# Kernel optimization log

Hardware: AMD Instinct MI355X
Metric: run time of the kernel (lower is better)

## Reference

```python
import jax, jax.numpy as jnp
import numpy as np

B, H, W, C = 2, 64, 64, 256
NH, K = 8, 7
HD = C // NH


def setup_inputs() -> dict:
    key = jax.random.key(0)
    ks = jax.random.split(key, 5)
    s = lambda fan: 1.0 / np.sqrt(fan)
    return {
        "x": jax.random.normal(ks[0], (B, H, W, C), jnp.float32),
        "ln1_w": jnp.ones((C,), jnp.float32),
        "ln1_b": jnp.zeros((C,), jnp.float32),
        "qkv_w": jax.random.normal(ks[1], (3 * C, C), jnp.float32) * s(C),
        "qkv_b": jnp.zeros((3 * C,), jnp.float32),
        "proj_w": jax.random.normal(ks[2], (C, C), jnp.float32) * s(C),
        "proj_b": jnp.zeros((C,), jnp.float32),
        "ln2_w": jnp.ones((C,), jnp.float32),
        "ln2_b": jnp.zeros((C,), jnp.float32),
        "fc1_w": jax.random.normal(ks[3], (4 * C, C), jnp.float32) * s(C),
        "fc1_b": jnp.zeros((4 * C,), jnp.float32),
        "fc2_w": jax.random.normal(ks[4], (C, 4 * C), jnp.float32) * s(4 * C),
        "fc2_b": jnp.zeros((C,), jnp.float32),
    }


def _ln(x, w, b, eps=1e-5):
    m = x.mean(-1, keepdims=True)
    v = ((x - m) ** 2).mean(-1, keepdims=True)
    return (x - m) * jax.lax.rsqrt(v + eps) * w + b


def _nbr_idx(n, k):
    # NATTEN non-causal window: start clamped so the full k-window fits in [0, n)
    half = k // 2
    start = np.clip(np.arange(n) - half, 0, n - k)
    return jnp.asarray(start[:, None] + np.arange(k)[None, :])  # [n, k]


def reference(x, ln1_w, ln1_b, qkv_w, qkv_b, proj_w, proj_b,
              ln2_w, ln2_b, fc1_w, fc1_b, fc2_w, fc2_b):
    shortcut = x
    xn = _ln(x, ln1_w, ln1_b)
    qkv = (xn @ qkv_w.T + qkv_b).reshape(B, H, W, 3, NH, HD)
    qkv = jnp.transpose(qkv, (3, 0, 4, 1, 2, 5))  # [3,B,NH,H,W,HD]
    q, k, v = qkv[0], qkv[1], qkv[2]
    q = q * (HD ** -0.5)
    ih = _nbr_idx(H, K)[:, None, :, None]   # [H,1,K,1]
    iw = _nbr_idx(W, K)[None, :, None, :]   # [1,W,1,K]
    # gather 7x7 neighborhoods -> [B,NH,H,W,K,K,HD] -> [B,NH,H,W,K*K,HD]
    k_nb = k[:, :, ih, iw, :].reshape(B, NH, H, W, K * K, HD)
    v_nb = v[:, :, ih, iw, :].reshape(B, NH, H, W, K * K, HD)
    attn = jnp.einsum("bnijd,bnijkd->bnijk", q, k_nb)  # na2d_qk
    attn = jax.nn.softmax(attn, axis=-1)
    out = jnp.einsum("bnijk,bnijkd->bnijd", attn, v_nb)  # na2d_av
    out = jnp.transpose(out, (0, 2, 3, 1, 4)).reshape(B, H, W, C)
    out = out @ proj_w.T + proj_b
    x = shortcut + out
    h = _ln(x, ln2_w, ln2_b)
    h = jax.nn.gelu(h @ fc1_w.T + fc1_b, approximate=False)
    h = h @ fc2_w.T + fc2_b
    return x + h
```

## Files before the change

kernel.cpp:

```cpp
#include <hip/hip_runtime.h>
#include <math.h>

#define Hdim 64
#define Wdim 64
#define NTOK 8192

typedef unsigned short ushortT;
typedef __attribute__((ext_vector_type(8))) short short8;
typedef __attribute__((ext_vector_type(4))) float floatx4;

__device__ inline ushortT f2bf(float x) {
    union { float f; unsigned u; } v; v.f = x;
    unsigned r = (v.u + 0x7fffu + ((v.u >> 16) & 1u)) >> 16;
    return (ushortT)r;
}

#define GLOAD_LDS16(g, l) __builtin_amdgcn_global_load_lds( \
    (const __attribute__((address_space(1))) unsigned int*)(g), \
    (__attribute__((address_space(3))) unsigned int*)(l), 16, 0, 0)

__global__ __launch_bounds__(256) void convert_weights(
        const float* __restrict__ qkv_w, const float* __restrict__ proj_w,
        const float* __restrict__ fc1_w, const float* __restrict__ fc2_w,
        ushortT* __restrict__ o_qkv, ushortT* __restrict__ o_proj,
        ushortT* __restrict__ o_fc1, ushortT* __restrict__ o_fc2) {
    int idx = blockIdx.x * 256 + threadIdx.x;
    const float* src; ushortT* dst; int local;
    if (idx < 49152)        { src = qkv_w;  dst = o_qkv;  local = idx; }
    else if (idx < 65536)   { src = proj_w; dst = o_proj; local = idx - 49152; }
    else if (idx < 131072)  { src = fc1_w;  dst = o_fc1;  local = idx - 65536; }
    else                    { src = fc2_w;  dst = o_fc2;  local = idx - 131072; }
    float4 v = ((const float4*)src)[local];
    ushortT o[4] = {f2bf(v.x), f2bf(v.y), f2bf(v.z), f2bf(v.w)};
    *(uint2*)(dst + (size_t)local * 4) = *(uint2*)o;
}

__global__ __launch_bounds__(256) void ln_v2(const float* __restrict__ x,
                                             const float* __restrict__ w,
                                             const float* __restrict__ b,
                                             ushortT* __restrict__ y) {
    int wave = threadIdx.x >> 6, lane = threadIdx.x & 63;
    int t = blockIdx.x * 4 + wave;
    float4 v = *(const float4*)(x + (size_t)t * 256 + lane * 4);
    float s = v.x + v.y + v.z + v.w;
    float sq = v.x * v.x + v.y * v.y + v.z * v.z + v.w * v.w;
#pragma unroll
    for (int off = 32; off > 0; off >>= 1) {
        s  += __shfl_xor(s, off, 64);
        sq += __shfl_xor(sq, off, 64);
    }
    float mean = s * (1.0f / 256.0f);
    float var  = sq * (1.0f / 256.0f) - mean * mean;
    float r = rsqrtf(var + 1e-5f);
    float4 wv = *(const float4*)(w + lane * 4);
    float4 bv = *(const float4*)(b + lane * 4);
    ushortT o[4] = {f2bf((v.x - mean) * r * wv.x + bv.x),
                    f2bf((v.y - mean) * r * wv.y + bv.y),
                    f2bf((v.z - mean) * r * wv.z + bv.z),
                    f2bf((v.w - mean) * r * wv.w + bv.w)};
    *(uint2*)(y + (size_t)t * 256 + lane * 4) = *(uint2*)o;
}

template <int EPI>
__global__ __launch_bounds__(256) void gemm_bf16_v2(const ushortT* __restrict__ A,
                                                    const ushortT* __restrict__ Bw,
                                                    const float* __restrict__ bias,
                                                    const float* __restrict__ res,
                                                    void* __restrict__ out0,
                                                    ushortT* __restrict__ kb,
                                                    ushortT* __restrict__ vb,
                                                    int N, int K) {
    __shared__ ushortT As[64 * 64];
    __shared__ ushortT Bs[64 * 64];
    const int tid  = threadIdx.x;
    const int wave = tid >> 6, lane = tid & 63;
    const int wm = wave >> 1, wn = wave & 1;
    const int ln16 = lane & 15, kg = lane >> 4;
    const int m0 = blockIdx.y * 64, n0 = blockIdx.x * 64;
    const int g8 = (((lane & 7) ^ (lane >> 3)) * 8);
    const int srow = wave * 16 + (lane >> 3);

    const floatx4 fzero = {0.f, 0.f, 0.f, 0.f};
    floatx4 acc[2][2];
#pragma unroll
    for (int i = 0; i < 2; ++i)
#pragma unroll
        for (int j = 0; j < 2; ++j) acc[i][j] = fzero;

    for (int kt = 0; kt < K; kt += 64) {
#pragma unroll
        for (int p = 0; p < 2; ++p) {
            int row = srow + p * 8;
            GLOAD_LDS16(A  + (size_t)(m0 + row) * K + kt + g8, As + wave * 1024 + p * 512);
            GLOAD_LDS16(Bw + (size_t)(n0 + row) * K + kt + g8, Bs + wave * 1024 + p * 512);
        }
        __syncthreads();
#pragma unroll
        for (int s = 0; s < 2; ++s) {
            short8 a[2], b[2];
#pragma unroll
            for (int i = 0; i < 2; ++i) {
                int ra = wm * 32 + i * 16 + ln16;
                a[i] = *(const short8*)(As + ra * 64 + (((s * 4 + kg) ^ (ra & 7)) * 8));
            }
#pragma unroll
            for (int j = 0; j < 2; ++j) {
                int rb = wn * 32 + j * 16 + ln16;
                b[j] = *(const short8*)(Bs + rb * 64 + (((s * 4 + kg) ^ (rb & 7)) * 8));
            }
#pragma unroll
            for (int i = 0; i < 2; ++i)
#pragma unroll
                for (int j = 0; j < 2; ++j)
                    acc[i][j] = __builtin_amdgcn_mfma_f32_16x16x32_bf16(a[i], b[j], acc[i][j], 0, 0, 0);
        }
        __syncthreads();
    }

#pragma unroll
    for (int j = 0; j < 2; ++j) {
        int col = n0 + wn * 32 + j * 16 + ln16;
        float bsv = bias[col];
        if (EPI == 0) {
            int part = col >> 8, h = (col >> 5) & 7, d = col & 31;
            ushortT* dst = part == 0 ? (ushortT*)out0 : (part == 1 ? kb : vb);
            float scl = part == 0 ? 0.17677669529663687f : 1.0f;
#pragma unroll
            for (int i = 0; i < 2; ++i)
#pragma unroll
                for (int r = 0; r < 4; ++r) {
                    int row = m0 + wm * 32 + i * 16 + kg * 4 + r;
                    int bI = row >> 12, tin = row & 4095;
                    dst[((size_t)(bI * 8 + h) * 4096 + tin) * 32 + d] =
                        f2bf((acc[i][j][r] + bsv) * scl);
                }
        } else {
#pragma unroll
            for (int i = 0; i < 2; ++i)
#pragma unroll
                for (int r = 0; r < 4; ++r) {
                    int row = m0 + wm * 32 + i * 16 + kg * 4 + r;
                    float v = acc[i][j][r] + bsv;
                    if (EPI == 1) {
                        v += res[(size_t)row * N + col];
                        ((float*)out0)[(size_t)row * N + col] = v;
                    } else {
                        v = 0.5f * v * (1.0f + erff(v * 0.70710678118654752f));
                        ((ushortT*)out0)[(size_t)row * N + col] = f2bf(v);
                    }
                }
        }
    }
}

__global__ __launch_bounds__(256) void natten_v3(const ushortT* __restrict__ qb,
                                                 const ushortT* __restrict__ kb,
                                                 const ushortT* __restrict__ vb,
                                                 ushortT* __restrict__ attn_out) {
    __shared__ ushortT KVs[2 * 196 * 40];
    __shared__ float Ps[64][52];
    ushortT* Ks = KVs;
    ushortT* Vs = KVs + 196 * 40;
    const int tid = threadIdx.x, bid = blockIdx.x;
    const int tile = bid & 63, h = (bid >> 6) & 7, b = bid >> 9;
    const int ti = tile >> 3, tj = tile & 7;
    const int r0 = min(max(ti * 8 - 3, 0), Hdim - 14);
    const int c0 = min(max(tj * 8 - 3, 0), Wdim - 14);
    const size_t base = (size_t)(b * 8 + h) * 4096 * 32;

    for (int idx = tid; idx < 1568; idx += 256) {
        int t = idx;
        const ushortT* src = kb;
        ushortT* dst = Ks;
        if (t >= 784) { t -= 784; src = vb; dst = Vs; }
        int pos = t >> 2, ch = t & 3;
        int dr = pos / 14, dc = pos - dr * 14;
        int tok = (r0 + dr) * 64 + (c0 + dc);
        *(uint4*)(dst + pos * 40 + ch * 8) = *(const uint4*)(src + base + (size_t)tok * 32 + ch * 8);
    }

    const int tl = tid >> 2, s = tid & 3;
    const int i = ti * 8 + (tl >> 3), j = tj * 8 + (tl & 7);
    const int si = min(max(i - 3, 0), Hdim - 7), sj = min(max(j - 3, 0), Wdim - 7);
    const int lbase = (si - r0) * 14 + (sj - c0);
    const int tin = i * 64 + j;

    float q[32];
    {
        const ushortT* qp = qb + base + (size_t)tin * 32;
#pragma unroll
        for (int c4 = 0; c4 < 4; ++c4) {
            uint4 u = *(const uint4*)(qp + c4 * 8);
            unsigned uu[4] = {u.x, u.y, u.z, u.w};
#pragma unroll
            for (int e = 0; e < 4; ++e) {
                union { unsigned v; float f; } lo, hi;
                lo.v = uu[e] << 16; hi.v = uu[e] & 0xffff0000u;
                q[c4 * 8 + e * 2] = lo.f; q[c4 * 8 + e * 2 + 1] = hi.f;
            }
        }
    }
    __syncthreads();

    float sc[13];
#pragma unroll
    for (int cI = 0; cI < 13; ++cI) {
        int n = s + cI * 4;
        if (n < 49) {
            int di = n / 7, dj = n - di * 7;
            const ushortT* kr = Ks + (lbase + di * 14 + dj) * 40;
            float a = 0.f;
#pragma unroll
            for (int c4 = 0; c4 < 4; ++c4) {
                uint4 u = *(const uint4*)(kr + c4 * 8);
                unsigned uu[4] = {u.x, u.y, u.z, u.w};
#pragma unroll
                for (int e = 0; e < 4; ++e) {
                    union { unsigned v; float f; } lo, hi;
                    lo.v = uu[e] << 16; hi.v = uu[e] & 0xffff0000u;
                    a += q[c4 * 8 + e * 2] * lo.f + q[c4 * 8 + e * 2 + 1] * hi.f;
                }
            }
            sc[cI] = a;
        }
    }
    float m = -1e30f;
#pragma unroll
    for (int cI = 0; cI < 13; ++cI) if (s + cI * 4 < 49) m = fmaxf(m, sc[cI]);
    m = fmaxf(m, __shfl_xor(m, 1, 64));
    m = fmaxf(m, __shfl_xor(m, 2, 64));
    float tot = 0.f;
#pragma unroll
    for (int cI = 0; cI < 13; ++cI) if (s + cI * 4 < 49) { sc[cI] = __expf(sc[cI] - m); tot += sc[cI]; }
    tot += __shfl_xor(tot, 1, 64);
    tot += __shfl_xor(tot, 2, 64);
    float inv = 1.0f / tot;
#pragma unroll
    for (int cI = 0; cI < 13; ++cI) if (s + cI * 4 < 49) Ps[tl][s + cI * 4] = sc[cI] * inv;
    __syncthreads();

    float o[8] = {0.f, 0.f, 0.f, 0.f, 0.f, 0.f, 0.f, 0.f};
#pragma unroll
    for (int n = 0; n < 49; ++n) {
        int di = n / 7, dj = n - di * 7;
        float p = Ps[tl][n];
        const ushortT* vr = Vs + (lbase + di * 14 + dj) * 40 + s * 8;
        uint4 u = *(const uint4*)vr;
        unsigned uu[4] = {u.x, u.y, u.z, u.w};
#pragma unroll
        for (int e = 0; e < 4; ++e) {
            union { unsigned v; float f; } lo, hi;
            lo.v = uu[e] << 16; hi.v = uu[e] & 0xffff0000u;
            o[e * 2]     += p * lo.f;
            o[e * 2 + 1] += p * hi.f;
        }
    }
    unsigned up[4];
#pragma unroll
    for (int d = 0; d < 4; ++d)
        up[d] = (unsigned)f2bf(o[2 * d]) | ((unsigned)f2bf(o[2 * d + 1]) << 16);
    size_t tq = (size_t)(b * 4096 + tin);
    *(uint4*)(attn_out + tq * 256 + h * 32 + s * 8) = make_uint4(up[0], up[1], up[2], up[3]);
}

extern "C" void kernel_launch(void* const* d_in, const int* in_sizes, int n_in,
                              void* d_out, int out_size, void* d_ws, size_t ws_size,
                              hipStream_t stream) {
    const float* x      = (const float*)d_in[0];
    const float* ln1_w  = (const float*)d_in[1];
    const float* ln1_b  = (const float*)d_in[2];
    const float* qkv_w  = (const float*)d_in[3];
    const float* qkv_b  = (const float*)d_in[4];
    const float* proj_w = (const float*)d_in[5];
    const float* proj_b = (const float*)d_in[6];
    const float* ln2_w  = (const float*)d_in[7];
    const float* ln2_b  = (const float*)d_in[8];
    const float* fc1_w  = (const float*)d_in[9];
    const float* fc1_b  = (const float*)d_in[10];
    const float* fc2_w  = (const float*)d_in[11];
    const float* fc2_b  = (const float*)d_in[12];
    float* out = (float*)d_out;

    char* ws = (char*)d_ws;
    size_t off = 0;
    ushortT* wqkv = (ushortT*)(ws + off); off += (size_t)196608 * 2;
    ushortT* wproj= (ushortT*)(ws + off); off += (size_t)65536 * 2;
    ushortT* wfc1 = (ushortT*)(ws + off); off += (size_t)262144 * 2;
    ushortT* wfc2 = (ushortT*)(ws + off); off += (size_t)262144 * 2;
    ushortT* xn   = (ushortT*)(ws + off); off += (size_t)NTOK * 256 * 2;
    ushortT* qbuf = (ushortT*)(ws + off); off += (size_t)NTOK * 256 * 2;
    ushortT* kbuf = (ushortT*)(ws + off); off += (size_t)NTOK * 256 * 2;
    ushortT* vbuf = (ushortT*)(ws + off); off += (size_t)NTOK * 256 * 2;
    ushortT* attn = (ushortT*)(ws + off); off += (size_t)NTOK * 256 * 2;
    float*   x2   = (float*)  (ws + off); off += (size_t)NTOK * 256 * 4;
    ushortT* hb   = (ushortT*)(ws + off); off += (size_t)NTOK * 256 * 2;
    ushortT* h1   = (ushortT*)(ws + off); off += (size_t)NTOK * 1024 * 2;

    dim3 blk(256);
    convert_weights<<<768, blk, 0, stream>>>(qkv_w, proj_w, fc1_w, fc2_w,
                                             wqkv, wproj, wfc1, wfc2);
    ln_v2<<<2048, blk, 0, stream>>>(x, ln1_w, ln1_b, xn);
    gemm_bf16_v2<0><<<dim3(12, 128), blk, 0, stream>>>(xn, wqkv, qkv_b, nullptr,
                                                       qbuf, kbuf, vbuf, 768, 256);
    natten_v3<<<1024, blk, 0, stream>>>(qbuf, kbuf, vbuf, attn);
    gemm_bf16_v2<1><<<dim3(4, 128), blk, 0, stream>>>(attn, wproj, proj_b, x,
                                                      x2, nullptr, nullptr, 256, 256);
    ln_v2<<<2048, blk, 0, stream>>>(x2, ln2_w, ln2_b, hb);
    gemm_bf16_v2<2><<<dim3(16, 128), blk, 0, stream>>>(hb, wfc1, fc1_b, nullptr,
                                                       h1, nullptr, nullptr, 1024, 256);
    gemm_bf16_v2<1><<<dim3(4, 128), blk, 0, stream>>>(h1, wfc2, fc2_b, x2,
                                                      out, nullptr, nullptr, 256, 1024);
}
```

Baseline: 153.7 us.

## Enlarge GEMM tiles to 128x128 and fuse weight conversion with first LayerNorm

The bf16 GEMM now uses 128x128 block tiles, with each wave computing a 64x64 sub-tile through 4x4 MFMA accumulators. This raises operand reuse per LDS load and cuts the number of blocks. Weight conversion and LN1 are merged into a single launch to save one kernel launch. The larger tile cuts grid sizes to as few as 128 blocks, which may leave CUs idle on the smaller GEMMs, and it increases register pressure.

```diff
diff --git a/kernel.cpp b/kernel.cpp
--- a/kernel.cpp
+++ b/kernel.cpp
@@ -19,20 +19,45 @@
     (const __attribute__((address_space(1))) unsigned int*)(g), \
     (__attribute__((address_space(3))) unsigned int*)(l), 16, 0, 0)
 
-__global__ __launch_bounds__(256) void convert_weights(
+__global__ __launch_bounds__(256) void prep_kernel(
         const float* __restrict__ qkv_w, const float* __restrict__ proj_w,
         const float* __restrict__ fc1_w, const float* __restrict__ fc2_w,
         ushortT* __restrict__ o_qkv, ushortT* __restrict__ o_proj,
-        ushortT* __restrict__ o_fc1, ushortT* __restrict__ o_fc2) {
-    int idx = blockIdx.x * 256 + threadIdx.x;
-    const float* src; ushortT* dst; int local;
-    if (idx < 49152)        { src = qkv_w;  dst = o_qkv;  local = idx; }
-    else if (idx < 65536)   { src = proj_w; dst = o_proj; local = idx - 49152; }
-    else if (idx < 131072)  { src = fc1_w;  dst = o_fc1;  local = idx - 65536; }
-    else                    { src = fc2_w;  dst = o_fc2;  local = idx - 131072; }
-    float4 v = ((const float4*)src)[local];
-    ushortT o[4] = {f2bf(v.x), f2bf(v.y), f2bf(v.z), f2bf(v.w)};
-    *(uint2*)(dst + (size_t)local * 4) = *(uint2*)o;
+        ushortT* __restrict__ o_fc1, ushortT* __restrict__ o_fc2,
+        const float* __restrict__ x, const float* __restrict__ ln1_w,
+        const float* __restrict__ ln1_b, ushortT* __restrict__ xn) {
+    if (blockIdx.x < 768) {
+        int idx = blockIdx.x * 256 + threadIdx.x;
+        const float* src; ushortT* dst; int local;
+        if (idx < 49152)        { src = qkv_w;  dst = o_qkv;  local = idx; }
+        else if (idx < 65536)   { src = proj_w; dst = o_proj; local = idx - 49152; }
+        else if (idx < 131072)  { src = fc1_w;  dst = o_fc1;  local = idx - 65536; }
+        else                    { src = fc2_w;  dst = o_fc2;  local = idx - 131072; }
+        float4 v = ((const float4*)src)[local];
+        ushortT o[4] = {f2bf(v.x), f2bf(v.y), f2bf(v.z), f2bf(v.w)};
+        *(uint2*)(dst + (size_t)local * 4) = *(uint2*)o;
+    } else {
+        int wave = threadIdx.x >> 6, lane = threadIdx.x & 63;
+        int t = (blockIdx.x - 768) * 4 + wave;
+        float4 v = *(const float4*)(x + (size_t)t * 256 + lane * 4);
+        float s = v.x + v.y + v.z + v.w;
+        float sq = v.x * v.x + v.y * v.y + v.z * v.z + v.w * v.w;
+#pragma unroll
+        for (int off = 32; off > 0; off >>= 1) {
+            s  += __shfl_xor(s, off, 64);
+            sq += __shfl_xor(sq, off, 64);
+        }
+        float mean = s * (1.0f / 256.0f);
+        float var  = sq * (1.0f / 256.0f) - mean * mean;
+        float r = rsqrtf(var + 1e-5f);
+        float4 wv = *(const float4*)(ln1_w + lane * 4);
+        float4 bv = *(const float4*)(ln1_b + lane * 4);
+        ushortT o[4] = {f2bf((v.x - mean) * r * wv.x + bv.x),
+                        f2bf((v.y - mean) * r * wv.y + bv.y),
+                        f2bf((v.z - mean) * r * wv.z + bv.z),
+                        f2bf((v.w - mean) * r * wv.w + bv.w)};
+        *(uint2*)(xn + (size_t)t * 256 + lane * 4) = *(uint2*)o;
+    }
 }
 
 __global__ __launch_bounds__(256) void ln_v2(const float* __restrict__ x,
@@ -62,7 +87,7 @@
 }
 
 template <int EPI>
-__global__ __launch_bounds__(256) void gemm_bf16_v2(const ushortT* __restrict__ A,
+__global__ __launch_bounds__(256) void gemm_bf16_v3(const ushortT* __restrict__ A,
                                                     const ushortT* __restrict__ Bw,
                                                     const float* __restrict__ bias,
                                                     const float* __restrict__ res,
@@ -70,76 +95,79 @@
                                                     ushortT* __restrict__ kb,
                                                     ushortT* __restrict__ vb,
                                                     int N, int K) {
-    __shared__ ushortT As[64 * 64];
-    __shared__ ushortT Bs[64 * 64];
+    __shared__ ushortT As[128 * 64];
+    __shared__ ushortT Bs[128 * 64];
     const int tid  = threadIdx.x;
     const int wave = tid >> 6, lane = tid & 63;
     const int wm = wave >> 1, wn = wave & 1;
     const int ln16 = lane & 15, kg = lane >> 4;
-    const int m0 = blockIdx.y * 64, n0 = blockIdx.x * 64;
-    const int g8 = (((lane & 7) ^ (lane >> 3)) * 8);
-    const int srow = wave * 16 + (lane >> 3);
+    const int m0 = blockIdx.y * 128, n0 = blockIdx.x * 128;
+
+    const int srow = tid >> 3;
+    const int spos = tid & 7;
+    const int sgc  = spos ^ (srow & 7);
 
     const floatx4 fzero = {0.f, 0.f, 0.f, 0.f};
-    floatx4 acc[2][2];
-#pragma unroll
-    for (int i = 0; i < 2; ++i)
-#pragma unroll
-        for (int j = 0; j < 2; ++j) acc[i][j] = fzero;
+    floatx4 acc[4][4];
+#pragma unroll
+    for (int i = 0; i < 4; ++i)
+#pragma unroll
+        for (int j = 0; j < 4; ++j) acc[i][j] = fzero;
 
     for (int kt = 0; kt < K; kt += 64) {
 #pragma unroll
-        for (int p = 0; p < 2; ++p) {
-            int row = srow + p * 8;
-            GLOAD_LDS16(A  + (size_t)(m0 + row) * K + kt + g8, As + wave * 1024 + p * 512);
-            GLOAD_LDS16(Bw + (size_t)(n0 + row) * K + kt + g8, Bs + wave * 1024 + p * 512);
+        for (int q = 0; q < 4; ++q) {
+            int row = q * 32 + srow;
+            GLOAD_LDS16(A  + (size_t)(m0 + row) * K + kt + sgc * 8, As + (q * 256 + tid - lane) * 8);
+            GLOAD_LDS16(Bw + (size_t)(n0 + row) * K + kt + sgc * 8, Bs + (q * 256 + tid - lane) * 8);
         }
         __syncthreads();
 #pragma unroll
         for (int s = 0; s < 2; ++s) {
-            short8 a[2], b[2];
-#pragma unroll
-            for (int i = 0; i < 2; ++i) {
-                int ra = wm * 32 + i * 16 + ln16;
-                a[i] = *(const short8*)(As + ra * 64 + (((s * 4 + kg) ^ (ra & 7)) * 8));
+            int c = s * 4 + kg;
+            short8 a[4], b[4];
+#pragma unroll
+            for (int i = 0; i < 4; ++i) {
+                int ra = wm * 64 + i * 16 + ln16;
+                a[i] = *(const short8*)(As + ra * 64 + ((c ^ (ra & 7)) * 8));
             }
 #pragma unroll
-            for (int j = 0; j < 2; ++j) {
-                int rb = wn * 32 + j * 16 + ln16;
-                b[j] = *(const short8*)(Bs + rb * 64 + (((s * 4 + kg) ^ (rb & 7)) * 8));
+            for (int j = 0; j < 4; ++j) {
+                int rb = wn * 64 + j * 16 + ln16;
+                b[j] = *(const short8*)(Bs + rb * 64 + ((c ^ (rb & 7)) * 8));
             }
 #pragma unroll
-            for (int i = 0; i < 2; ++i)
-#pragma unroll
-                for (int j = 0; j < 2; ++j)
+            for (int i = 0; i < 4; ++i)
+#pragma unroll
+                for (int j = 0; j < 4; ++j)
                     acc[i][j] = __builtin_amdgcn_mfma_f32_16x16x32_bf16(a[i], b[j], acc[i][j], 0, 0, 0);
         }
         __syncthreads();
     }
 
 #pragma unroll
-    for (int j = 0; j < 2; ++j) {
-        int col = n0 + wn * 32 + j * 16 + ln16;
+    for (int j = 0; j < 4; ++j) {
+        int col = n0 + wn * 64 + j * 16 + ln16;
         float bsv = bias[col];
         if (EPI == 0) {
             int part = col >> 8, h = (col >> 5) & 7, d = col & 31;
             ushortT* dst = part == 0 ? (ushortT*)out0 : (part == 1 ? kb : vb);
             float scl = part == 0 ? 0.17677669529663687f : 1.0f;
 #pragma unroll
-            for (int i = 0; i < 2; ++i)
+            for (int i = 0; i < 4; ++i)
 #pragma unroll
                 for (int r = 0; r < 4; ++r) {
-                    int row = m0 + wm * 32 + i * 16 + kg * 4 + r;
+                    int row = m0 + wm * 64 + i * 16 + kg * 4 + r;
                     int bI = row >> 12, tin = row & 4095;
                     dst[((size_t)(bI * 8 + h) * 4096 + tin) * 32 + d] =
                         f2bf((acc[i][j][r] + bsv) * scl);
                 }
         } else {
 #pragma unroll
-            for (int i = 0; i < 2; ++i)
+            for (int i = 0; i < 4; ++i)
 #pragma unroll
                 for (int r = 0; r < 4; ++r) {
-                    int row = m0 + wm * 32 + i * 16 + kg * 4 + r;
+                    int row = m0 + wm * 64 + i * 16 + kg * 4 + r;
                     float v = acc[i][j][r] + bsv;
                     if (EPI == 1) {
                         v += res[(size_t)row * N + col];
@@ -297,17 +325,17 @@
     ushortT* h1   = (ushortT*)(ws + off); off += (size_t)NTOK * 1024 * 2;
 
     dim3 blk(256);
-    convert_weights<<<768, blk, 0, stream>>>(qkv_w, proj_w, fc1_w, fc2_w,
-                                             wqkv, wproj, wfc1, wfc2);
-    ln_v2<<<2048, blk, 0, stream>>>(x, ln1_w, ln1_b, xn);
-    gemm_bf16_v2<0><<<dim3(12, 128), blk, 0, stream>>>(xn, wqkv, qkv_b, nullptr,
-                                                       qbuf, kbuf, vbuf, 768, 256);
+    prep_kernel<<<2816, blk, 0, stream>>>(qkv_w, proj_w, fc1_w, fc2_w,
+                                          wqkv, wproj, wfc1, wfc2,
+                                          x, ln1_w, ln1_b, xn);
+    gemm_bf16_v3<0><<<dim3(6, 64), blk, 0, stream>>>(xn, wqkv, qkv_b, nullptr,
+                                                     qbuf, kbuf, vbuf, 768, 256);
     natten_v3<<<1024, blk, 0, stream>>>(qbuf, kbuf, vbuf, attn);
-    gemm_bf16_v2<1><<<dim3(4, 128), blk, 0, stream>>>(attn, wproj, proj_b, x,
-                                                      x2, nullptr, nullptr, 256, 256);
+    gemm_bf16_v3<1><<<dim3(2, 64), blk, 0, stream>>>(attn, wproj, proj_b, x,
+                                                     x2, nullptr, nullptr, 256, 256);
     ln_v2<<<2048, blk, 0, stream>>>(x2, ln2_w, ln2_b, hb);
-    gemm_bf16_v2<2><<<dim3(16, 128), blk, 0, stream>>>(hb, wfc1, fc1_b, nullptr,
-                                                       h1, nullptr, nullptr, 1024, 256);
-    gemm_bf16_v2<1><<<dim3(4, 128), blk, 0, stream>>>(h1, wfc2, fc2_b, x2,
-                                                      out, nullptr, nullptr, 256, 1024);
-}
+    gemm_bf16_v3<2><<<dim3(8, 64), blk, 0, stream>>>(hb, wfc1, fc1_b, nullptr,
+                                                     h1, nullptr, nullptr, 1024, 256);
+    gemm_bf16_v3<1><<<dim3(2, 64), blk, 0, stream>>>(h1, wfc2, fc2_b, x2,
+                                                     out, nullptr, nullptr, 256, 1024);
+}
```

New measurement: 167.1 us. 8.7% more time.

## Merge weight conversion with first LayerNorm and use skinny-tile GEMM for N=256 outputs

Applied to the files above, without the earlier changes.

Folds the weight bf16 conversion and the first LayerNorm into one launch, saving a kernel launch and letting the two independent jobs overlap. Adds a 32x64-tile GEMM for the proj and fc2 projections (N=256), doubling the block count from 512 to 1024 so more CUs are busy, with the residual add kept in its epilogue. The trade-off is that each block reuses less data, and the skinny kernel has no double buffering and a full sync on every K step.

```diff
diff --git a/kernel.cpp b/kernel.cpp
--- a/kernel.cpp
+++ b/kernel.cpp
@@ -19,20 +19,45 @@
     (const __attribute__((address_space(1))) unsigned int*)(g), \
     (__attribute__((address_space(3))) unsigned int*)(l), 16, 0, 0)
 
-__global__ __launch_bounds__(256) void convert_weights(
+__global__ __launch_bounds__(256) void prep_kernel(
         const float* __restrict__ qkv_w, const float* __restrict__ proj_w,
         const float* __restrict__ fc1_w, const float* __restrict__ fc2_w,
         ushortT* __restrict__ o_qkv, ushortT* __restrict__ o_proj,
-        ushortT* __restrict__ o_fc1, ushortT* __restrict__ o_fc2) {
-    int idx = blockIdx.x * 256 + threadIdx.x;
-    const float* src; ushortT* dst; int local;
-    if (idx < 49152)        { src = qkv_w;  dst = o_qkv;  local = idx; }
-    else if (idx < 65536)   { src = proj_w; dst = o_proj; local = idx - 49152; }
-    else if (idx < 131072)  { src = fc1_w;  dst = o_fc1;  local = idx - 65536; }
-    else                    { src = fc2_w;  dst = o_fc2;  local = idx - 131072; }
-    float4 v = ((const float4*)src)[local];
-    ushortT o[4] = {f2bf(v.x), f2bf(v.y), f2bf(v.z), f2bf(v.w)};
-    *(uint2*)(dst + (size_t)local * 4) = *(uint2*)o;
+        ushortT* __restrict__ o_fc1, ushortT* __restrict__ o_fc2,
+        const float* __restrict__ x, const float* __restrict__ ln1_w,
+        const float* __restrict__ ln1_b, ushortT* __restrict__ xn) {
+    if (blockIdx.x < 768) {
+        int idx = blockIdx.x * 256 + threadIdx.x;
+        const float* src; ushortT* dst; int local;
+        if (idx < 49152)        { src = qkv_w;  dst = o_qkv;  local = idx; }
+        else if (idx < 65536)   { src = proj_w; dst = o_proj; local = idx - 49152; }
+        else if (idx < 131072)  { src = fc1_w;  dst = o_fc1;  local = idx - 65536; }
+        else                    { src = fc2_w;  dst = o_fc2;  local = idx - 131072; }
+        float4 v = ((const float4*)src)[local];
+        ushortT o[4] = {f2bf(v.x), f2bf(v.y), f2bf(v.z), f2bf(v.w)};
+        *(uint2*)(dst + (size_t)local * 4) = *(uint2*)o;
+    } else {
+        int wave = threadIdx.x >> 6, lane = threadIdx.x & 63;
+        int t = (blockIdx.x - 768) * 4 + wave;
+        float4 v = *(const float4*)(x + (size_t)t * 256 + lane * 4);
+        float s = v.x + v.y + v.z + v.w;
+        float sq = v.x * v.x + v.y * v.y + v.z * v.z + v.w * v.w;
+#pragma unroll
+        for (int off = 32; off > 0; off >>= 1) {
+            s  += __shfl_xor(s, off, 64);
+            sq += __shfl_xor(sq, off, 64);
+        }
+        float mean = s * (1.0f / 256.0f);
+        float var  = sq * (1.0f / 256.0f) - mean * mean;
+        float r = rsqrtf(var + 1e-5f);
+        float4 wv = *(const float4*)(ln1_w + lane * 4);
+        float4 bv = *(const float4*)(ln1_b + lane * 4);
+        ushortT o[4] = {f2bf((v.x - mean) * r * wv.x + bv.x),
+                        f2bf((v.y - mean) * r * wv.y + bv.y),
+                        f2bf((v.z - mean) * r * wv.z + bv.z),
+                        f2bf((v.w - mean) * r * wv.w + bv.w)};
+        *(uint2*)(xn + (size_t)t * 256 + lane * 4) = *(uint2*)o;
+    }
 }
 
 __global__ __launch_bounds__(256) void ln_v2(const float* __restrict__ x,
@@ -65,7 +90,6 @@
 __global__ __launch_bounds__(256) void gemm_bf16_v2(const ushortT* __restrict__ A,
                                                     const ushortT* __restrict__ Bw,
                                                     const float* __restrict__ bias,
-                                                    const float* __restrict__ res,
                                                     void* __restrict__ out0,
                                                     ushortT* __restrict__ kb,
                                                     ushortT* __restrict__ vb,
@@ -141,14 +165,68 @@
                 for (int r = 0; r < 4; ++r) {
                     int row = m0 + wm * 32 + i * 16 + kg * 4 + r;
                     float v = acc[i][j][r] + bsv;
-                    if (EPI == 1) {
-                        v += res[(size_t)row * N + col];
-                        ((float*)out0)[(size_t)row * N + col] = v;
-                    } else {
-                        v = 0.5f * v * (1.0f + erff(v * 0.70710678118654752f));
-                        ((ushortT*)out0)[(size_t)row * N + col] = f2bf(v);
-                    }
+                    v = 0.5f * v * (1.0f + erff(v * 0.70710678118654752f));
+                    ((ushortT*)out0)[(size_t)row * N + col] = f2bf(v);
                 }
+        }
+    }
+}
+
+__global__ __launch_bounds__(256) void gemm_skinny(const ushortT* __restrict__ A,
+                                                   const ushortT* __restrict__ Bw,
+                                                   const float* __restrict__ bias,
+                                                   const float* __restrict__ res,
+                                                   float* __restrict__ out,
+                                                   int K) {
+    __shared__ ushortT As[32 * 64];
+    __shared__ ushortT Bs[64 * 64];
+    const int tid  = threadIdx.x;
+    const int wave = tid >> 6, lane = tid & 63;
+    const int wm = wave >> 1, wn = wave & 1;
+    const int ln16 = lane & 15, kg = lane >> 4;
+    const int m0 = blockIdx.y * 32, n0 = blockIdx.x * 64;
+    const int srow = tid >> 3;
+    const int spos = tid & 7;
+    const int sgc  = spos ^ (srow & 7);
+    const int brow = wave * 16 + (lane >> 3);
+    const int bg8  = (((lane & 7) ^ (lane >> 3)) * 8);
+
+    const floatx4 fzero = {0.f, 0.f, 0.f, 0.f};
+    floatx4 acc[2] = {fzero, fzero};
+
+    for (int kt = 0; kt < K; kt += 64) {
+        GLOAD_LDS16(A + (size_t)(m0 + srow) * K + kt + sgc * 8, As + (tid - lane) * 8);
+#pragma unroll
+        for (int p = 0; p < 2; ++p) {
+            int row = brow + p * 8;
+            GLOAD_LDS16(Bw + (size_t)(n0 + row) * K + kt + bg8, Bs + wave * 1024 + p * 512);
+        }
+        __syncthreads();
+#pragma unroll
+        for (int s = 0; s < 2; ++s) {
+            int c = s * 4 + kg;
+            int ra = wm * 16 + ln16;
+            short8 a = *(const short8*)(As + ra * 64 + ((c ^ (ra & 7)) * 8));
+            short8 b[2];
+#pragma unroll
+            for (int j = 0; j < 2; ++j) {
+                int rb = wn * 32 + j * 16 + ln16;
+                b[j] = *(const short8*)(Bs + rb * 64 + ((c ^ (rb & 7)) * 8));
+            }
+            acc[0] = __builtin_amdgcn_mfma_f32_16x16x32_bf16(a, b[0], acc[0], 0, 0, 0);
+            acc[1] = __builtin_amdgcn_mfma_f32_16x16x32_bf16(a, b[1], acc[1], 0, 0, 0);
+        }
+        __syncthreads();
+    }
+
+#pragma unroll
+    for (int j = 0; j < 2; ++j) {
+        int col = n0 + wn * 32 + j * 16 + ln16;
+        float bsv = bias[col];
+#pragma unroll
+        for (int r = 0; r < 4; ++r) {
+            int row = m0 + wm * 16 + kg * 4 + r;
+            out[(size_t)row * 256 + col] = acc[j][r] + bsv + res[(size_t)row * 256 + col];
         }
     }
 }
@@ -297,17 +375,15 @@
     ushortT* h1   = (ushortT*)(ws + off); off += (size_t)NTOK * 1024 * 2;
 
     dim3 blk(256);
-    convert_weights<<<768, blk, 0, stream>>>(qkv_w, proj_w, fc1_w, fc2_w,
-                                             wqkv, wproj, wfc1, wfc2);
-    ln_v2<<<2048, blk, 0, stream>>>(x, ln1_w, ln1_b, xn);
-    gemm_bf16_v2<0><<<dim3(12, 128), blk, 0, stream>>>(xn, wqkv, qkv_b, nullptr,
+    prep_kernel<<<2816, blk, 0, stream>>>(qkv_w, proj_w, fc1_w, fc2_w,
+                                          wqkv, wproj, wfc1, wfc2,
+                                          x, ln1_w, ln1_b, xn);
+    gemm_bf16_v2<0><<<dim3(12, 128), blk, 0, stream>>>(xn, wqkv, qkv_b,
                                                        qbuf, kbuf, vbuf, 768, 256);
     natten_v3<<<1024, blk, 0, stream>>>(qbuf, kbuf, vbuf, attn);
-    gemm_bf16_v2<1><<<dim3(4, 128), blk, 0, stream>>>(attn, wproj, proj_b, x,
-                                                      x2, nullptr, nullptr, 256, 256);
+    gemm_skinny<<<dim3(4, 256), blk, 0, stream>>>(attn, wproj, proj_b, x, x2, 256);
     ln_v2<<<2048, blk, 0, stream>>>(x2, ln2_w, ln2_b, hb);
-    gemm_bf16_v2<2><<<dim3(16, 128), blk, 0, stream>>>(hb, wfc1, fc1_b, nullptr,
+    gemm_bf16_v2<2><<<dim3(16, 128), blk, 0, stream>>>(hb, wfc1, fc1_b,
                                                        h1, nullptr, nullptr, 1024, 256);
-    gemm_bf16_v2<1><<<dim3(4, 128), blk, 0, stream>>>(h1, wfc2, fc2_b, x2,
-                                                      out, nullptr, nullptr, 256, 1024);
-}
+    gemm_skinny<<<dim3(4, 256), blk, 0, stream>>>(h1, wfc2, fc2_b, x2, out, 1024);
+}
```

Result: no change. 151.5 us (-1.5%).
